# Kernel tuning notes

Hardware: AMD Instinct MI355X
Metric: run time of the kernel (lower is better)

## Reference

```python
import jax, jax.numpy as jnp
import numpy as np

N_BLOCKS = 9
D = 256  # input_dim == edge_dim == hidden_dim
N_NODES = 10000
N_EDGES = 60000
LN_EPS = 1e-5


def _layer_norm(h, g, b):
    m = h.mean(-1, keepdims=True)
    v = ((h - m) ** 2).mean(-1, keepdims=True)
    return (h - m) * jax.lax.rsqrt(v + LN_EPS) * g + b


def _mlp(h, W1, b1, W2, b2, W3, b3, g, beta):
    # Linear->ReLU, Linear->ReLU (hidden_layers=2), Linear, LayerNorm
    h = jax.nn.relu(h @ W1 + b1)
    h = jax.nn.relu(h @ W2 + b2)
    h = h @ W3 + b3
    return _layer_norm(h, g, beta)


def setup_inputs() -> dict:
    key = jax.random.key(0)
    ks = jax.random.split(key, 24)
    x = jax.random.normal(ks[0], (N_NODES, D), jnp.float32)
    edge_index = jax.random.randint(ks[1], (2, N_EDGES), 0, N_NODES, jnp.int32)
    edge_attr = jax.random.normal(ks[2], (N_EDGES, D), jnp.float32)

    def w(k, shape):
        fan_in = shape[-2]
        return jax.random.normal(k, shape, jnp.float32) * (1.0 / np.sqrt(fan_in))

    B = N_BLOCKS
    inp = {"x": x, "edge_index": edge_index, "edge_attr": edge_attr}
    # edge MLP: in 3D -> D -> D -> D, LayerNorm(D)
    inp["eW1"] = w(ks[3], (B, 3 * D, D)); inp["eB1"] = jnp.zeros((B, D), jnp.float32)
    inp["eW2"] = w(ks[4], (B, D, D));     inp["eB2"] = jnp.zeros((B, D), jnp.float32)
    inp["eW3"] = w(ks[5], (B, D, D));     inp["eB3"] = jnp.zeros((B, D), jnp.float32)
    inp["eLNg"] = jnp.ones((B, D), jnp.float32); inp["eLNb"] = jnp.zeros((B, D), jnp.float32)
    # node MLP: in 2D -> D -> D -> D, LayerNorm(D)
    inp["nW1"] = w(ks[6], (B, 2 * D, D)); inp["nB1"] = jnp.zeros((B, D), jnp.float32)
    inp["nW2"] = w(ks[7], (B, D, D));     inp["nB2"] = jnp.zeros((B, D), jnp.float32)
    inp["nW3"] = w(ks[8], (B, D, D));     inp["nB3"] = jnp.zeros((B, D), jnp.float32)
    inp["nLNg"] = jnp.ones((B, D), jnp.float32); inp["nLNb"] = jnp.zeros((B, D), jnp.float32)
    return inp


def reference(x, edge_index, edge_attr,
              eW1, eB1, eW2, eB2, eW3, eB3, eLNg, eLNb,
              nW1, nB1, nW2, nB2, nW3, nB3, nLNg, nLNb):
    src = edge_index[0]
    dst = edge_index[1]
    n_nodes = x.shape[0]

    def block(carry, p):
        xc, ea = carry
        (ew1, eb1, ew2, eb2, ew3, eb3, eg, ebn,
         nw1, nb1, nw2, nb2, nw3, nb3, ng, nbn) = p
        # edge update: gather endpoints, MLP, residual
        msg_in = jnp.concatenate([xc[src], xc[dst], ea], axis=-1)  # [E, 3D]
        ea = ea + _mlp(msg_in, ew1, eb1, ew2, eb2, ew3, eb3, eg, ebn)
        # node update: scatter-sum messages to destination, MLP, residual
        agg = jax.ops.segment_sum(ea, dst, num_segments=n_nodes)  # [N, D]
        node_in = jnp.concatenate([xc, agg], axis=-1)  # [N, 2D]
        xc = xc + _mlp(node_in, nw1, nb1, nw2, nb2, nw3, nb3, ng, nbn)
        return (xc, ea), None

    params = (eW1, eB1, eW2, eB2, eW3, eB3, eLNg, eLNb,
              nW1, nB1, nW2, nB2, nW3, nB3, nLNg, nLNb)
    (x_out, _), _ = jax.lax.scan(block, (x, edge_attr), params)
    return x_out
```

## Files before the change

### kernel.cpp

```cpp
#include <hip/hip_runtime.h>

#define D 256

typedef __attribute__((ext_vector_type(8))) short bf16x8;
typedef __attribute__((ext_vector_type(4))) float f32x4;

__device__ inline unsigned short f2bf(float f) {
  union { float f; unsigned u; } v; v.f = f;
  unsigned r = v.u + 0x7FFFu + ((v.u >> 16) & 1u);
  return (unsigned short)(r >> 16);
}
__device__ inline float bf2f(unsigned short u) {
  union { unsigned u; float f; } v; v.u = ((unsigned)u) << 16;
  return v.f;
}

__device__ inline void gl_lds16(const void* gsrc, void* ldst) {
  __builtin_amdgcn_global_load_lds(
      (const __attribute__((address_space(1))) void*)gsrc,
      (__attribute__((address_space(3))) void*)ldst, 16, 0, 0);
}

__global__ void wprep_kernel(const float* __restrict__ w, unsigned short* __restrict__ wt,
                             int Kfull, int k0, int Ksub, int total) {
  int idx = blockIdx.x * 256 + threadIdx.x;
  if (idx >= total) return;
  int per_b = Ksub * D;
  int b = idx / per_b;
  int r = idx % per_b;
  int j = r & 7;
  int lane = (r >> 3) & 63;
  int t = r >> 9;
  int kt = t >> 4, ct = t & 15;
  int k = kt * 32 + (lane >> 4) * 8 + j;
  int col = ct * 16 + (lane & 15);
  wt[idx] = f2bf(w[((size_t)b * Kfull + k0 + k) * D + col]);
}

__global__ void cvt_bf16_kernel(const float4* __restrict__ in, ushort4* __restrict__ out, int n4) {
  int i = blockIdx.x * 256 + threadIdx.x;
  if (i >= n4) return;
  float4 f = in[i];
  ushort4 o;
  o.x = f2bf(f.x); o.y = f2bf(f.y); o.z = f2bf(f.z); o.w = f2bf(f.w);
  out[i] = o;
}

__global__ void hist_kernel(const int* __restrict__ dst, int* __restrict__ hist, int E) {
  int i = blockIdx.x * 256 + threadIdx.x;
  if (i < E) atomicAdd(&hist[dst[i]], 1);
}

__global__ void scan_kernel(const int* __restrict__ hist, int* __restrict__ offs, int Nn) {
  __shared__ int part[256];
  int t = threadIdx.x;
  int chunk = (Nn + 255) >> 8;
  int s = t * chunk;
  int e = s + chunk; if (e > Nn) e = Nn; if (s > Nn) s = Nn;
  int sum = 0;
  for (int i = s; i < e; ++i) sum += hist[i];
  part[t] = sum;
  __syncthreads();
  if (t == 0) {
    int run = 0;
    for (int i = 0; i < 256; ++i) { int v = part[i]; part[i] = run; run += v; }
  }
  __syncthreads();
  int run = part[t];
  for (int i = s; i < e; ++i) { offs[i] = run; run += hist[i]; }
  if (e == Nn) offs[Nn] = run;
}

__global__ void fill_kernel(const int* __restrict__ dst, const int* __restrict__ offs,
                            int* __restrict__ cnt, int* __restrict__ eid, int E) {
  int i = blockIdx.x * 256 + threadIdx.x;
  if (i < E) {
    int d = dst[i];
    int p = offs[d] + atomicAdd(&cnt[d], 1);
    eid[p] = i;
  }
}

__global__ __launch_bounds__(256) void agg_kernel(
    const unsigned short* __restrict__ eabf, const int* __restrict__ eid,
    const int* __restrict__ offs, unsigned short* __restrict__ aggbf, int Nn) {
  int node = blockIdx.x * 4 + (threadIdx.x >> 6);
  if (node >= Nn) return;
  int lane = threadIdx.x & 63;
  int s = offs[node], e = offs[node + 1];
  float4 acc = make_float4(0.f, 0.f, 0.f, 0.f);
  for (int i = s; i < e; ++i) {
    int ed = eid[i];
    ushort4 v = *(const ushort4*)(eabf + (size_t)ed * D + lane * 4);
    acc.x += bf2f(v.x); acc.y += bf2f(v.y); acc.z += bf2f(v.z); acc.w += bf2f(v.w);
  }
  ushort4 o;
  o.x = f2bf(acc.x); o.y = f2bf(acc.y); o.z = f2bf(acc.z); o.w = f2bf(acc.w);
  *(ushort4*)(aggbf + (size_t)node * D + lane * 4) = o;
}

__global__ __launch_bounds__(256, 4) void gemm32(
    const unsigned short* __restrict__ A, const unsigned short* __restrict__ W,
    unsigned short* __restrict__ out, int M)
{
  const int tid  = threadIdx.x;
  const int lane = tid & 63;
  const int wave = tid >> 6;
  const int lr   = lane & 15;
  const int lq   = lane >> 4;
  const int r0   = blockIdx.x * 32;

  int ro[2];
  #pragma unroll
  for (int mt = 0; mt < 2; ++mt) {
    int rw = r0 + mt * 16 + lr;
    if (rw > M - 1) rw = M - 1;
    ro[mt] = rw * D;
  }
  const int ctb = wave * 4;
  f32x4 acc[2][4];
  #pragma unroll
  for (int i = 0; i < 2; i++)
    #pragma unroll
    for (int j = 0; j < 4; j++)
      acc[i][j] = (f32x4){0.f, 0.f, 0.f, 0.f};

  constexpr int DEPTH = 3;
  bf16x8 afb[DEPTH][2], bqb[DEPTH][4];
  #pragma unroll
  for (int d = 0; d < DEPTH; ++d) {
    #pragma unroll
    for (int mt = 0; mt < 2; ++mt)
      afb[d][mt] = *(const bf16x8*)(A + ro[mt] + (d << 5) + lq * 8);
    #pragma unroll
    for (int nt = 0; nt < 4; ++nt)
      bqb[d][nt] = *(const bf16x8*)(W + (((d * 16 + ctb + nt) * 64 + lane) * 8));
  }
  #pragma unroll
  for (int kt = 0; kt < 8; ++kt) {
    const int s = kt % DEPTH;
    #pragma unroll
    for (int mt = 0; mt < 2; ++mt)
      #pragma unroll
      for (int nt = 0; nt < 4; ++nt)
        acc[mt][nt] = __builtin_amdgcn_mfma_f32_16x16x32_bf16(afb[s][mt], bqb[s][nt], acc[mt][nt], 0, 0, 0);
    if (kt + DEPTH < 8) {
      const int kn = kt + DEPTH;
      #pragma unroll
      for (int mt = 0; mt < 2; ++mt)
        afb[s][mt] = *(const bf16x8*)(A + ro[mt] + (kn << 5) + lq * 8);
      #pragma unroll
      for (int nt = 0; nt < 4; ++nt)
        bqb[s][nt] = *(const bf16x8*)(W + (((kn * 16 + ctb + nt) * 64 + lane) * 8));
    }
  }
  #pragma unroll
  for (int mt = 0; mt < 2; ++mt)
    #pragma unroll
    for (int r = 0; r < 4; ++r) {
      const int row = r0 + mt * 16 + lq * 4 + r;
      if (row < M) {
        #pragma unroll
        for (int nt = 0; nt < 4; ++nt)
          out[(size_t)row * D + wave * 64 + nt * 16 + lr] = f2bf(acc[mt][nt][r]);
      }
    }
}

__global__ __launch_bounds__(256, 4) void fused_edge(
    unsigned short* __restrict__ eabf,
    const int* __restrict__ src, const int* __restrict__ dst,
    const unsigned short* __restrict__ Ubf, const unsigned short* __restrict__ Vbf,
    const unsigned short* __restrict__ W1c, const float* __restrict__ b1,
    const unsigned short* __restrict__ W2, const float* __restrict__ b2,
    const unsigned short* __restrict__ W3, const float* __restrict__ b3,
    const float* __restrict__ lng, const float* __restrict__ lnb, int E)
{
  __shared__ __align__(16) unsigned short SH[16896];
  unsigned short* Us = SH;
  unsigned short* Vs = SH + 8192;
  unsigned short* Hs = SH;
  float* ps1 = (float*)(SH + 16384);
  float* ps2 = (float*)(SH + 16384) + 128;

  const int tid  = threadIdx.x;
  const int lane = tid & 63;
  const int wave = tid >> 6;
  const int lr   = lane & 15;
  const int lq   = lane >> 4;
  const int r0   = blockIdx.x * 32;

  #pragma unroll
  for (int c = 0; c < 4; ++c) {
    int row = wave * 8 + c * 2 + (lane >> 5);
    int er = r0 + row; if (er > E - 1) er = E - 1;
    int colel = (lane & 31) * 8;
    gl_lds16(Ubf + (size_t)src[er] * D + colel, Us + wave * 2048 + c * 512);
    gl_lds16(Vbf + (size_t)dst[er] * D + colel, Vs + wave * 2048 + c * 512);
  }

  int ro[2];
  #pragma unroll
  for (int mt = 0; mt < 2; ++mt) {
    int rw = r0 + mt * 16 + lr;
    if (rw > E - 1) rw = E - 1;
    ro[mt] = rw * D;
  }
  const int ctb = wave * 4;
  #define LOADB(Wp, kt, dst_)                                                 \
    _Pragma("unroll")                                                         \
    for (int nt = 0; nt < 4; ++nt)                                            \
      dst_[nt] = *(const bf16x8*)((Wp) + ((((kt) * 16 + ctb + nt) * 64 + lane) * 8));

  f32x4 acc[2][4];
  constexpr int DEPTH = 3;
  bf16x8 afb[DEPTH][2], bqb[DEPTH][4];

  #pragma unroll
  for (int i = 0; i < 2; i++)
    #pragma unroll
    for (int j = 0; j < 4; j++)
      acc[i][j] = (f32x4){0.f, 0.f, 0.f, 0.f};
  #pragma unroll
  for (int d = 0; d < DEPTH; ++d) {
    #pragma unroll
    for (int mt = 0; mt < 2; ++mt)
      afb[d][mt] = *(const bf16x8*)(eabf + ro[mt] + (d << 5) + lq * 8);
    LOADB(W1c, d, bqb[d]);
  }
  #pragma unroll
  for (int kt = 0; kt < 8; ++kt) {
    const int s = kt % DEPTH;
    #pragma unroll
    for (int mt = 0; mt < 2; ++mt)
      #pragma unroll
      for (int nt = 0; nt < 4; ++nt)
        acc[mt][nt] = __builtin_amdgcn_mfma_f32_16x16x32_bf16(afb[s][mt], bqb[s][nt], acc[mt][nt], 0, 0, 0);
    if (kt + DEPTH < 8) {
      const int kn = kt + DEPTH;
      #pragma unroll
      for (int mt = 0; mt < 2; ++mt)
        afb[s][mt] = *(const bf16x8*)(eabf + ro[mt] + (kn << 5) + lq * 8);
      LOADB(W1c, kn, bqb[s]);
    }
  }
  __syncthreads();

  {
    float bv[4];
    #pragma unroll
    for (int nt = 0; nt < 4; ++nt) bv[nt] = b1[wave * 64 + nt * 16 + lr];
    #pragma unroll
    for (int mt = 0; mt < 2; ++mt)
      #pragma unroll
      for (int r = 0; r < 4; ++r) {
        const int row = mt * 16 + lq * 4 + r;
        #pragma unroll
        for (int nt = 0; nt < 4; ++nt) {
          const int col = wave * 64 + nt * 16 + lr;
          float v = acc[mt][nt][r] + bv[nt]
                  + bf2f(Us[row * 256 + col]) + bf2f(Vs[row * 256 + col]);
          acc[mt][nt][r] = v > 0.f ? v : 0.f;
        }
      }
  }
  __syncthreads();
  #pragma unroll
  for (int mt = 0; mt < 2; ++mt)
    #pragma unroll
    for (int r = 0; r < 4; ++r) {
      const int row = mt * 16 + lq * 4 + r;
      #pragma unroll
      for (int nt = 0; nt < 4; ++nt)
        Hs[row * 264 + wave * 64 + nt * 16 + lr] = f2bf(acc[mt][nt][r]);
    }
  __syncthreads();

  #pragma unroll
  for (int i = 0; i < 2; i++)
    #pragma unroll
    for (int j = 0; j < 4; j++)
      acc[i][j] = (f32x4){0.f, 0.f, 0.f, 0.f};
  #pragma unroll
  for (int d = 0; d < DEPTH; ++d) LOADB(W2, d, bqb[d]);
  #pragma unroll
  for (int kt = 0; kt < 8; ++kt) {
    const int s = kt % DEPTH;
    bf16x8 afc[2];
    #pragma unroll
    for (int mt = 0; mt < 2; ++mt)
      afc[mt] = *(const bf16x8*)&Hs[(mt * 16 + lr) * 264 + (kt << 5) + lq * 8];
    #pragma unroll
    for (int mt = 0; mt < 2; ++mt)
      #pragma unroll
      for (int nt = 0; nt < 4; ++nt)
        acc[mt][nt] = __builtin_amdgcn_mfma_f32_16x16x32_bf16(afc[mt], bqb[s][nt], acc[mt][nt], 0, 0, 0);
    if (kt + DEPTH < 8) LOADB(W2, kt + DEPTH, bqb[s]);
  }
  __syncthreads();
  {
    float bv[4];
    #pragma unroll
    for (int nt = 0; nt < 4; ++nt) bv[nt] = b2[wave * 64 + nt * 16 + lr];
    #pragma unroll
    for (int mt = 0; mt < 2; ++mt)
      #pragma unroll
      for (int r = 0; r < 4; ++r) {
        const int row = mt * 16 + lq * 4 + r;
        #pragma unroll
        for (int nt = 0; nt < 4; ++nt) {
          float v = acc[mt][nt][r] + bv[nt];
          v = v > 0.f ? v : 0.f;
          Hs[row * 264 + wave * 64 + nt * 16 + lr] = f2bf(v);
        }
      }
  }
  __syncthreads();

  #pragma unroll
  for (int i = 0; i < 2; i++)
    #pragma unroll
    for (int j = 0; j < 4; j++)
      acc[i][j] = (f32x4){0.f, 0.f, 0.f, 0.f};
  #pragma unroll
  for (int d = 0; d < DEPTH; ++d) LOADB(W3, d, bqb[d]);
  #pragma unroll
  for (int kt = 0; kt < 8; ++kt) {
    const int s = kt % DEPTH;
    bf16x8 afc[2];
    #pragma unroll
    for (int mt = 0; mt < 2; ++mt)
      afc[mt] = *(const bf16x8*)&Hs[(mt * 16 + lr) * 264 + (kt << 5) + lq * 8];
    #pragma unroll
    for (int mt = 0; mt < 2; ++mt)
      #pragma unroll
      for (int nt = 0; nt < 4; ++nt)
        acc[mt][nt] = __builtin_amdgcn_mfma_f32_16x16x32_bf16(afc[mt], bqb[s][nt], acc[mt][nt], 0, 0, 0);
    if (kt + DEPTH < 8) LOADB(W3, kt + DEPTH, bqb[s]);
  }
  #pragma unroll
  for (int nt = 0; nt < 4; ++nt) {
    const float bv = b3[wave * 64 + nt * 16 + lr];
    #pragma unroll
    for (int mt = 0; mt < 2; ++mt)
      #pragma unroll
      for (int r = 0; r < 4; ++r)
        acc[mt][nt][r] += bv;
  }
  #pragma unroll
  for (int mt = 0; mt < 2; ++mt) {
    #pragma unroll
    for (int r = 0; r < 4; ++r) {
      float s1 = 0.f, s2 = 0.f;
      #pragma unroll
      for (int nt = 0; nt < 4; ++nt) {
        float v = acc[mt][nt][r];
        s1 += v; s2 += v * v;
      }
      #pragma unroll
      for (int dlt = 1; dlt < 16; dlt <<= 1) {
        s1 += __shfl_xor(s1, dlt, 64);
        s2 += __shfl_xor(s2, dlt, 64);
      }
      if (lr == 0) {
        ps1[(mt * 16 + lq * 4 + r) * 4 + wave] = s1;
        ps2[(mt * 16 + lq * 4 + r) * 4 + wave] = s2;
      }
    }
  }
  __syncthreads();
  #pragma unroll
  for (int mt = 0; mt < 2; ++mt) {
    #pragma unroll
    for (int r = 0; r < 4; ++r) {
      const int rl = mt * 16 + lq * 4 + r;
      const int row = r0 + rl;
      float fs1 = ps1[rl * 4 + 0] + ps1[rl * 4 + 1] + ps1[rl * 4 + 2] + ps1[rl * 4 + 3];
      float fs2 = ps2[rl * 4 + 0] + ps2[rl * 4 + 1] + ps2[rl * 4 + 2] + ps2[rl * 4 + 3];
      float mean = fs1 * (1.f / 256.f);
      float var  = fs2 * (1.f / 256.f) - mean * mean;
      float rstd = rsqrtf(var + 1e-5f);
      if (row < E) {
        #pragma unroll
        for (int nt = 0; nt < 4; ++nt) {
          const int col = wave * 64 + nt * 16 + lr;
          float v = (acc[mt][nt][r] - mean) * rstd * lng[col] + lnb[col];
          unsigned short* bp = eabf + (size_t)row * D + col;
          *bp = f2bf(bf2f(*bp) + v);
        }
      }
    }
  }
  #undef LOADB
}

template<int NCHUNK>
__global__ __launch_bounds__(256, 4) void fused_mlp(
    const unsigned short* __restrict__ C0, const int* __restrict__ g0,
    const unsigned short* __restrict__ C1, const int* __restrict__ g1,
    const unsigned short* __restrict__ C2,
    const unsigned short* __restrict__ W1, const float* __restrict__ b1,
    const unsigned short* __restrict__ W2, const float* __restrict__ b2,
    const unsigned short* __restrict__ W3, const float* __restrict__ b3,
    const float* __restrict__ lng, const float* __restrict__ lnb,
    float* __restrict__ resid, unsigned short* __restrict__ bfout, int M)
{
  __shared__ __align__(16) unsigned short Hs[32 * 264];
  __shared__ float ps1[128];
  __shared__ float ps2[128];

  const int tid  = threadIdx.x;
  const int lane = tid & 63;
  const int wave = tid >> 6;
  const int lr   = lane & 15;
  const int lq   = lane >> 4;
  const int r0   = blockIdx.x * 32;

  int ro0[2], ro1[2], ro2[2];
  #pragma unroll
  for (int mt = 0; mt < 2; ++mt) {
    int rw = r0 + mt * 16 + lr;
    if (rw > M - 1) rw = M - 1;
    ro0[mt] = (g0 ? g0[rw] : rw) * D;
    ro1[mt] = (NCHUNK > 1) ? ((g1 ? g1[rw] : rw) * D) : 0;
    ro2[mt] = (NCHUNK > 2) ? rw * D : 0;
  }

  f32x4 acc[2][4];
  const int ctb = wave * 4;
  #define LOADB(Wp, kt, dst)                                                  \
    _Pragma("unroll")                                                         \
    for (int nt = 0; nt < 4; ++nt)                                            \
      dst[nt] = *(const bf16x8*)((Wp) + ((((kt) * 16 + ctb + nt) * 64 + lane) * 8));
  #define LOADA(kt, dst) {                                                    \
    const int c_ = (kt) >> 3;                                                 \
    const int koff_ = (((kt) & 7) << 5) + lq * 8;                             \
    const unsigned short* bp_ = (c_ == 0) ? C0 : (c_ == 1 ? C1 : C2);         \
    _Pragma("unroll")                                                         \
    for (int mt = 0; mt < 2; ++mt) {                                          \
      int r_ = ro0[mt];                                                       \
      if (NCHUNK > 1 && c_ == 1) r_ = ro1[mt];                                \
      if (NCHUNK > 2 && c_ == 2) r_ = ro2[mt];                                \
      dst[mt] = *(const bf16x8*)(bp_ + r_ + koff_);                           \
    }                                                                         \
  }

  constexpr int DEPTH = 3;
  bf16x8 afb[DEPTH][2], bqb[DEPTH][4];

  #pragma unroll
  for (int i = 0; i < 2; i++)
    #pragma unroll
    for (int j = 0; j < 4; j++)
      acc[i][j] = (f32x4){0.f, 0.f, 0.f, 0.f};

  constexpr int NKT = NCHUNK * 8;
  #pragma unroll
  for (int d = 0; d < DEPTH; ++d) {
    LOADA(d, afb[d]);
    LOADB(W1, d, bqb[d]);
  }
  #pragma unroll
  for (int kt = 0; kt < NKT; ++kt) {
    const int s = kt % DEPTH;
    #pragma unroll
    for (int mt = 0; mt < 2; ++mt)
      #pragma unroll
      for (int nt = 0; nt < 4; ++nt)
        acc[mt][nt] = __builtin_amdgcn_mfma_f32_16x16x32_bf16(afb[s][mt], bqb[s][nt], acc[mt][nt], 0, 0, 0);
    if (kt + DEPTH < NKT) {
      LOADA(kt + DEPTH, afb[s]);
      LOADB(W1, kt + DEPTH, bqb[s]);
    }
  }
  {
    float bv[4];
    #pragma unroll
    for (int nt = 0; nt < 4; ++nt) bv[nt] = b1[wave * 64 + nt * 16 + lr];
    #pragma unroll
    for (int mt = 0; mt < 2; ++mt)
      #pragma unroll
      for (int r = 0; r < 4; ++r) {
        const int row = mt * 16 + lq * 4 + r;
        #pragma unroll
        for (int nt = 0; nt < 4; ++nt) {
          float v = acc[mt][nt][r] + bv[nt];
          v = v > 0.f ? v : 0.f;
          Hs[row * 264 + wave * 64 + nt * 16 + lr] = f2bf(v);
        }
      }
  }
  __syncthreads();

  #pragma unroll
  for (int i = 0; i < 2; i++)
    #pragma unroll
    for (int j = 0; j < 4; j++)
      acc[i][j] = (f32x4){0.f, 0.f, 0.f, 0.f};
  #pragma unroll
  for (int d = 0; d < DEPTH; ++d) LOADB(W2, d, bqb[d]);
  #pragma unroll
  for (int kt = 0; kt < 8; ++kt) {
    const int s = kt % DEPTH;
    bf16x8 afc[2];
    #pragma unroll
    for (int mt = 0; mt < 2; ++mt)
      afc[mt] = *(const bf16x8*)&Hs[(mt * 16 + lr) * 264 + (kt << 5) + lq * 8];
    #pragma unroll
    for (int mt = 0; mt < 2; ++mt)
      #pragma unroll
      for (int nt = 0; nt < 4; ++nt)
        acc[mt][nt] = __builtin_amdgcn_mfma_f32_16x16x32_bf16(afc[mt], bqb[s][nt], acc[mt][nt], 0, 0, 0);
    if (kt + DEPTH < 8) LOADB(W2, kt + DEPTH, bqb[s]);
  }
  __syncthreads();
  {
    float bv[4];
    #pragma unroll
    for (int nt = 0; nt < 4; ++nt) bv[nt] = b2[wave * 64 + nt * 16 + lr];
    #pragma unroll
    for (int mt = 0; mt < 2; ++mt)
      #pragma unroll
      for (int r = 0; r < 4; ++r) {
        const int row = mt * 16 + lq * 4 + r;
        #pragma unroll
        for (int nt = 0; nt < 4; ++nt) {
          float v = acc[mt][nt][r] + bv[nt];
          v = v > 0.f ? v : 0.f;
          Hs[row * 264 + wave * 64 + nt * 16 + lr] = f2bf(v);
        }
      }
  }
  __syncthreads();

  #pragma unroll
  for (int i = 0; i < 2; i++)
    #pragma unroll
    for (int j = 0; j < 4; j++)
      acc[i][j] = (f32x4){0.f, 0.f, 0.f, 0.f};
  #pragma unroll
  for (int d = 0; d < DEPTH; ++d) LOADB(W3, d, bqb[d]);
  #pragma unroll
  for (int kt = 0; kt < 8; ++kt) {
    const int s = kt % DEPTH;
    bf16x8 afc[2];
    #pragma unroll
    for (int mt = 0; mt < 2; ++mt)
      afc[mt] = *(const bf16x8*)&Hs[(mt * 16 + lr) * 264 + (kt << 5) + lq * 8];
    #pragma unroll
    for (int mt = 0; mt < 2; ++mt)
      #pragma unroll
      for (int nt = 0; nt < 4; ++nt)
        acc[mt][nt] = __builtin_amdgcn_mfma_f32_16x16x32_bf16(afc[mt], bqb[s][nt], acc[mt][nt], 0, 0, 0);
    if (kt + DEPTH < 8) LOADB(W3, kt + DEPTH, bqb[s]);
  }
  #pragma unroll
  for (int nt = 0; nt < 4; ++nt) {
    const float bv = b3[wave * 64 + nt * 16 + lr];
    #pragma unroll
    for (int mt = 0; mt < 2; ++mt)
      #pragma unroll
      for (int r = 0; r < 4; ++r)
        acc[mt][nt][r] += bv;
  }
  #pragma unroll
  for (int mt = 0; mt < 2; ++mt) {
    #pragma unroll
    for (int r = 0; r < 4; ++r) {
      float s1 = 0.f, s2 = 0.f;
      #pragma unroll
      for (int nt = 0; nt < 4; ++nt) {
        float v = acc[mt][nt][r];
        s1 += v; s2 += v * v;
      }
      #pragma unroll
      for (int dlt = 1; dlt < 16; dlt <<= 1) {
        s1 += __shfl_xor(s1, dlt, 64);
        s2 += __shfl_xor(s2, dlt, 64);
      }
      if (lr == 0) {
        ps1[(mt * 16 + lq * 4 + r) * 4 + wave] = s1;
        ps2[(mt * 16 + lq * 4 + r) * 4 + wave] = s2;
      }
    }
  }
  __syncthreads();
  #pragma unroll
  for (int mt = 0; mt < 2; ++mt) {
    #pragma unroll
    for (int r = 0; r < 4; ++r) {
      const int rl = mt * 16 + lq * 4 + r;
      const int row = r0 + rl;
      float fs1 = ps1[rl * 4 + 0] + ps1[rl * 4 + 1] + ps1[rl * 4 + 2] + ps1[rl * 4 + 3];
      float fs2 = ps2[rl * 4 + 0] + ps2[rl * 4 + 1] + ps2[rl * 4 + 2] + ps2[rl * 4 + 3];
      float mean = fs1 * (1.f / 256.f);
      float var  = fs2 * (1.f / 256.f) - mean * mean;
      float rstd = rsqrtf(var + 1e-5f);
      if (row < M) {
        #pragma unroll
        for (int nt = 0; nt < 4; ++nt) {
          const int col = wave * 64 + nt * 16 + lr;
          float v = (acc[mt][nt][r] - mean) * rstd * lng[col] + lnb[col];
          if (resid) {
            float* rp = resid + (size_t)row * D + col;
            float nv = *rp + v;
            *rp = nv;
            if (bfout) bfout[(size_t)row * D + col] = f2bf(nv);
          } else {
            unsigned short* bp = bfout + (size_t)row * D + col;
            *bp = f2bf(bf2f(*bp) + v);
          }
        }
      }
    }
  }
  #undef LOADA
  #undef LOADB
}

extern "C" void kernel_launch(void* const* d_in, const int* in_sizes, int n_in,
                              void* d_out, int out_size, void* d_ws, size_t ws_size,
                              hipStream_t stream) {
  const float* x         = (const float*)d_in[0];
  const int*   eidx      = (const int*)d_in[1];
  const float* edge_attr = (const float*)d_in[2];
  const float* eW1 = (const float*)d_in[3];
  const float* eB1 = (const float*)d_in[4];
  const float* eW2 = (const float*)d_in[5];
  const float* eB2 = (const float*)d_in[6];
  const float* eW3 = (const float*)d_in[7];
  const float* eB3 = (const float*)d_in[8];
  const float* eLNg = (const float*)d_in[9];
  const float* eLNb = (const float*)d_in[10];
  const float* nW1 = (const float*)d_in[11];
  const float* nB1 = (const float*)d_in[12];
  const float* nW2 = (const float*)d_in[13];
  const float* nB2 = (const float*)d_in[14];
  const float* nW3 = (const float*)d_in[15];
  const float* nB3 = (const float*)d_in[16];
  const float* nLNg = (const float*)d_in[17];
  const float* nLNb = (const float*)d_in[18];

  const int Nn = in_sizes[0] / D;
  const int E  = in_sizes[1] / 2;
  const int B  = in_sizes[4] / D;

  const int* srcI = eidx;
  const int* dstI = eidx + E;

  char* wsp = (char*)d_ws;
  size_t off = 0;
  auto alloc = [&](size_t bytes) {
    char* p = wsp + off;
    off += (bytes + 255) & ~(size_t)255;
    return p;
  };
  unsigned short* eW1at = (unsigned short*)alloc((size_t)B * 256 * D * 2);
  unsigned short* eW1bt = (unsigned short*)alloc((size_t)B * 256 * D * 2);
  unsigned short* eW1ct = (unsigned short*)alloc((size_t)B * 256 * D * 2);
  unsigned short* eW2t  = (unsigned short*)alloc((size_t)B * 256 * D * 2);
  unsigned short* eW3t  = (unsigned short*)alloc((size_t)B * 256 * D * 2);
  unsigned short* nW1t  = (unsigned short*)alloc((size_t)B * 512 * D * 2);
  unsigned short* nW2t  = (unsigned short*)alloc((size_t)B * 256 * D * 2);
  unsigned short* nW3t  = (unsigned short*)alloc((size_t)B * 256 * D * 2);
  unsigned short* eabf  = (unsigned short*)alloc((size_t)E * D * 2);
  unsigned short* xbf   = (unsigned short*)alloc((size_t)Nn * D * 2);
  unsigned short* aggbf = (unsigned short*)alloc((size_t)Nn * D * 2);
  unsigned short* Ubf   = (unsigned short*)alloc((size_t)Nn * D * 2);
  unsigned short* Vbf   = (unsigned short*)alloc((size_t)Nn * D * 2);
  int*            hist  = (int*)alloc((size_t)(Nn + 1) * 4);
  int*            offs  = (int*)alloc((size_t)(Nn + 1) * 4);
  int*            cnt   = (int*)alloc((size_t)Nn * 4);
  int*            eid   = (int*)alloc((size_t)E * 4);

  float* xbuf = (float*)d_out;

  auto wp = [&](const float* w, unsigned short* wt, int Kfull, int k0, int Ksub) {
    int total = B * Ksub * D;
    wprep_kernel<<<(total + 255) / 256, 256, 0, stream>>>(w, wt, Kfull, k0, Ksub, total);
  };
  wp(eW1, eW1at, 768, 0, 256);
  wp(eW1, eW1bt, 768, 256, 256);
  wp(eW1, eW1ct, 768, 512, 256);
  wp(eW2, eW2t, 256, 0, 256);
  wp(eW3, eW3t, 256, 0, 256);
  wp(nW1, nW1t, 512, 0, 512);
  wp(nW2, nW2t, 256, 0, 256);
  wp(nW3, nW3t, 256, 0, 256);

  hipMemcpyAsync(xbuf, x, (size_t)Nn * D * 4, hipMemcpyDeviceToDevice, stream);
  {
    int n4 = E * D / 4;
    cvt_bf16_kernel<<<(n4 + 255) / 256, 256, 0, stream>>>(
        (const float4*)edge_attr, (ushort4*)eabf, n4);
    int m4 = Nn * D / 4;
    cvt_bf16_kernel<<<(m4 + 255) / 256, 256, 0, stream>>>(
        (const float4*)x, (ushort4*)xbf, m4);
  }

  hipMemsetAsync(hist, 0, (size_t)Nn * 4, stream);
  hipMemsetAsync(cnt, 0, (size_t)Nn * 4, stream);
  hist_kernel<<<(E + 255) / 256, 256, 0, stream>>>(dstI, hist, E);
  scan_kernel<<<1, 256, 0, stream>>>(hist, offs, Nn);
  fill_kernel<<<(E + 255) / 256, 256, 0, stream>>>(dstI, offs, cnt, eid, E);

  const int gridE = (E + 31) / 32;
  const int gridN = (Nn + 31) / 32;
  const int gridA = (Nn + 3) / 4;

  for (int b = 0; b < B; ++b) {
    gemm32<<<gridN, 256, 0, stream>>>(xbf, eW1at + (size_t)b * 256 * D, Ubf, Nn);
    gemm32<<<gridN, 256, 0, stream>>>(xbf, eW1bt + (size_t)b * 256 * D, Vbf, Nn);
    fused_edge<<<gridE, 256, 0, stream>>>(
        eabf, srcI, dstI, Ubf, Vbf,
        eW1ct + (size_t)b * 256 * D, eB1 + b * D,
        eW2t + (size_t)b * 256 * D, eB2 + b * D,
        eW3t + (size_t)b * 256 * D, eB3 + b * D,
        eLNg + b * D, eLNb + b * D, E);
    agg_kernel<<<gridA, 256, 0, stream>>>(eabf, eid, offs, aggbf, Nn);
    fused_mlp<2><<<gridN, 256, 0, stream>>>(
        xbf, nullptr, aggbf, nullptr, nullptr,
        nW1t + (size_t)b * 512 * D, nB1 + b * D,
        nW2t + (size_t)b * 256 * D, nB2 + b * D,
        nW3t + (size_t)b * 256 * D, nB3 + b * D,
        nLNg + b * D, nLNb + b * D, xbuf, xbf, Nn);
  }
}
```

Baseline: 1.384 ms.

## Merge U/V GEMMs, shrink node tiles to 16 rows, stage edge attrs in LDS

The two per-block node GEMMs for U and V become one launch that picks the weight and output by block index. The node GEMMs and the node MLP now use 16-row tiles, doubling grid size to improve occupancy on the 10k-node problem. The edge kernel stages its edge-attribute tile into padded LDS with coalesced loads and reads A fragments from there. Its residual update now goes through LDS and is written back with vectorized 16-byte stores instead of scattered 2-byte read-modify-writes. In exchange the edge kernel uses more LDS, which may lower occupancy, and the smaller node tiles reuse each weight load across fewer rows.

```diff
diff --git a/kernel.cpp b/kernel.cpp
--- a/kernel.cpp
+++ b/kernel.cpp
@@ -99,39 +99,35 @@
   *(ushort4*)(aggbf + (size_t)node * D + lane * 4) = o;
 }
 
-__global__ __launch_bounds__(256, 4) void gemm32(
-    const unsigned short* __restrict__ A, const unsigned short* __restrict__ W,
-    unsigned short* __restrict__ out, int M)
+__global__ __launch_bounds__(256, 4) void gemm_uv(
+    const unsigned short* __restrict__ A,
+    const unsigned short* __restrict__ Wa, const unsigned short* __restrict__ Wb,
+    unsigned short* __restrict__ U, unsigned short* __restrict__ V, int M)
 {
+  const int u    = blockIdx.x & 1;
+  const int r0   = (blockIdx.x >> 1) * 16;
+  const unsigned short* W = u ? Wb : Wa;
+  unsigned short* out = u ? V : U;
+
   const int tid  = threadIdx.x;
   const int lane = tid & 63;
   const int wave = tid >> 6;
   const int lr   = lane & 15;
   const int lq   = lane >> 4;
-  const int r0   = blockIdx.x * 32;
-
-  int ro[2];
-  #pragma unroll
-  for (int mt = 0; mt < 2; ++mt) {
-    int rw = r0 + mt * 16 + lr;
-    if (rw > M - 1) rw = M - 1;
-    ro[mt] = rw * D;
-  }
+
+  int rw = r0 + lr; if (rw > M - 1) rw = M - 1;
+  const int ro = rw * D;
   const int ctb = wave * 4;
-  f32x4 acc[2][4];
-  #pragma unroll
-  for (int i = 0; i < 2; i++)
-    #pragma unroll
-    for (int j = 0; j < 4; j++)
-      acc[i][j] = (f32x4){0.f, 0.f, 0.f, 0.f};
+
+  f32x4 acc[4];
+  #pragma unroll
+  for (int j = 0; j < 4; j++) acc[j] = (f32x4){0.f, 0.f, 0.f, 0.f};
 
   constexpr int DEPTH = 3;
-  bf16x8 afb[DEPTH][2], bqb[DEPTH][4];
+  bf16x8 afb[DEPTH], bqb[DEPTH][4];
   #pragma unroll
   for (int d = 0; d < DEPTH; ++d) {
-    #pragma unroll
-    for (int mt = 0; mt < 2; ++mt)
-      afb[d][mt] = *(const bf16x8*)(A + ro[mt] + (d << 5) + lq * 8);
+    afb[d] = *(const bf16x8*)(A + ro + (d << 5) + lq * 8);
     #pragma unroll
     for (int nt = 0; nt < 4; ++nt)
       bqb[d][nt] = *(const bf16x8*)(W + (((d * 16 + ctb + nt) * 64 + lane) * 8));
@@ -140,31 +136,25 @@
   for (int kt = 0; kt < 8; ++kt) {
     const int s = kt % DEPTH;
     #pragma unroll
-    for (int mt = 0; mt < 2; ++mt)
-      #pragma unroll
-      for (int nt = 0; nt < 4; ++nt)
-        acc[mt][nt] = __builtin_amdgcn_mfma_f32_16x16x32_bf16(afb[s][mt], bqb[s][nt], acc[mt][nt], 0, 0, 0);
+    for (int nt = 0; nt < 4; ++nt)
+      acc[nt] = __builtin_amdgcn_mfma_f32_16x16x32_bf16(afb[s], bqb[s][nt], acc[nt], 0, 0, 0);
     if (kt + DEPTH < 8) {
       const int kn = kt + DEPTH;
-      #pragma unroll
-      for (int mt = 0; mt < 2; ++mt)
-        afb[s][mt] = *(const bf16x8*)(A + ro[mt] + (kn << 5) + lq * 8);
+      afb[s] = *(const bf16x8*)(A + ro + (kn << 5) + lq * 8);
       #pragma unroll
       for (int nt = 0; nt < 4; ++nt)
         bqb[s][nt] = *(const bf16x8*)(W + (((kn * 16 + ctb + nt) * 64 + lane) * 8));
     }
   }
   #pragma unroll
-  for (int mt = 0; mt < 2; ++mt)
-    #pragma unroll
-    for (int r = 0; r < 4; ++r) {
-      const int row = r0 + mt * 16 + lq * 4 + r;
-      if (row < M) {
-        #pragma unroll
-        for (int nt = 0; nt < 4; ++nt)
-          out[(size_t)row * D + wave * 64 + nt * 16 + lr] = f2bf(acc[mt][nt][r]);
-      }
-    }
+  for (int r = 0; r < 4; ++r) {
+    const int row = r0 + lq * 4 + r;
+    if (row < M) {
+      #pragma unroll
+      for (int nt = 0; nt < 4; ++nt)
+        out[(size_t)row * D + wave * 64 + nt * 16 + lr] = f2bf(acc[nt][r]);
+    }
+  }
 }
 
 __global__ __launch_bounds__(256, 4) void fused_edge(
@@ -176,12 +166,13 @@
     const unsigned short* __restrict__ W3, const float* __restrict__ b3,
     const float* __restrict__ lng, const float* __restrict__ lnb, int E)
 {
-  __shared__ __align__(16) unsigned short SH[16896];
-  unsigned short* Us = SH;
-  unsigned short* Vs = SH + 8192;
-  unsigned short* Hs = SH;
-  float* ps1 = (float*)(SH + 16384);
-  float* ps2 = (float*)(SH + 16384) + 128;
+  __shared__ __align__(16) unsigned short SH[24832];
+  unsigned short* eaS = SH;
+  unsigned short* Hs  = SH;
+  unsigned short* Us  = SH + 8448;
+  unsigned short* Vs  = SH + 8448 + 8192;
+  float* ps1 = (float*)(SH + 8448);
+  float* ps2 = (float*)(SH + 8448) + 128;
 
   const int tid  = threadIdx.x;
   const int lane = tid & 63;
@@ -191,6 +182,16 @@
   const int r0   = blockIdx.x * 32;
 
   #pragma unroll
+  for (int i = 0; i < 4; ++i) {
+    int row = i * 8 + (tid >> 5);
+    int cs  = (tid & 31) * 8;
+    int er = r0 + row; if (er > E - 1) er = E - 1;
+    uint4 v = *(const uint4*)(eabf + (size_t)er * D + cs);
+    *(uint4*)&eaS[row * 264 + cs] = v;
+  }
+  __syncthreads();
+
+  #pragma unroll
   for (int c = 0; c < 4; ++c) {
     int row = wave * 8 + c * 2 + (lane >> 5);
     int er = r0 + row; if (er > E - 1) er = E - 1;
@@ -199,13 +200,6 @@
     gl_lds16(Vbf + (size_t)dst[er] * D + colel, Vs + wave * 2048 + c * 512);
   }
 
-  int ro[2];
-  #pragma unroll
-  for (int mt = 0; mt < 2; ++mt) {
-    int rw = r0 + mt * 16 + lr;
-    if (rw > E - 1) rw = E - 1;
-    ro[mt] = rw * D;
-  }
   const int ctb = wave * 4;
   #define LOADB(Wp, kt, dst_)                                                 \
     _Pragma("unroll")                                                         \
@@ -214,7 +208,7 @@
 
   f32x4 acc[2][4];
   constexpr int DEPTH = 3;
-  bf16x8 afb[DEPTH][2], bqb[DEPTH][4];
+  bf16x8 bqb[DEPTH][4];
 
   #pragma unroll
   for (int i = 0; i < 2; i++)
@@ -222,27 +216,20 @@
     for (int j = 0; j < 4; j++)
       acc[i][j] = (f32x4){0.f, 0.f, 0.f, 0.f};
   #pragma unroll
-  for (int d = 0; d < DEPTH; ++d) {
-    #pragma unroll
-    for (int mt = 0; mt < 2; ++mt)
-      afb[d][mt] = *(const bf16x8*)(eabf + ro[mt] + (d << 5) + lq * 8);
-    LOADB(W1c, d, bqb[d]);
-  }
+  for (int d = 0; d < DEPTH; ++d) LOADB(W1c, d, bqb[d]);
   #pragma unroll
   for (int kt = 0; kt < 8; ++kt) {
     const int s = kt % DEPTH;
+    bf16x8 afc[2];
+    #pragma unroll
+    for (int mt = 0; mt < 2; ++mt)
+      afc[mt] = *(const bf16x8*)&eaS[(mt * 16 + lr) * 264 + (kt << 5) + lq * 8];
     #pragma unroll
     for (int mt = 0; mt < 2; ++mt)
       #pragma unroll
       for (int nt = 0; nt < 4; ++nt)
-        acc[mt][nt] = __builtin_amdgcn_mfma_f32_16x16x32_bf16(afb[s][mt], bqb[s][nt], acc[mt][nt], 0, 0, 0);
-    if (kt + DEPTH < 8) {
-      const int kn = kt + DEPTH;
-      #pragma unroll
-      for (int mt = 0; mt < 2; ++mt)
-        afb[s][mt] = *(const bf16x8*)(eabf + ro[mt] + (kn << 5) + lq * 8);
-      LOADB(W1c, kn, bqb[s]);
-    }
+        acc[mt][nt] = __builtin_amdgcn_mfma_f32_16x16x32_bf16(afc[mt], bqb[s][nt], acc[mt][nt], 0, 0, 0);
+    if (kt + DEPTH < 8) LOADB(W1c, kt + DEPTH, bqb[s]);
   }
   __syncthreads();
 
@@ -374,103 +361,90 @@
     #pragma unroll
     for (int r = 0; r < 4; ++r) {
       const int rl = mt * 16 + lq * 4 + r;
-      const int row = r0 + rl;
       float fs1 = ps1[rl * 4 + 0] + ps1[rl * 4 + 1] + ps1[rl * 4 + 2] + ps1[rl * 4 + 3];
       float fs2 = ps2[rl * 4 + 0] + ps2[rl * 4 + 1] + ps2[rl * 4 + 2] + ps2[rl * 4 + 3];
       float mean = fs1 * (1.f / 256.f);
       float var  = fs2 * (1.f / 256.f) - mean * mean;
       float rstd = rsqrtf(var + 1e-5f);
-      if (row < E) {
-        #pragma unroll
-        for (int nt = 0; nt < 4; ++nt) {
-          const int col = wave * 64 + nt * 16 + lr;
-          float v = (acc[mt][nt][r] - mean) * rstd * lng[col] + lnb[col];
-          unsigned short* bp = eabf + (size_t)row * D + col;
-          *bp = f2bf(bf2f(*bp) + v);
-        }
-      }
+      #pragma unroll
+      for (int nt = 0; nt < 4; ++nt) {
+        const int col = wave * 64 + nt * 16 + lr;
+        float v = (acc[mt][nt][r] - mean) * rstd * lng[col] + lnb[col];
+        Hs[rl * 264 + col] = f2bf(v);
+      }
+    }
+  }
+  __syncthreads();
+  #pragma unroll
+  for (int i = 0; i < 4; ++i) {
+    int row = i * 8 + (tid >> 5);
+    int cs  = (tid & 31) * 8;
+    int er = r0 + row;
+    if (er < E) {
+      uint4 dv = *(const uint4*)&Hs[row * 264 + cs];
+      uint4 ov = *(const uint4*)(eabf + (size_t)er * D + cs);
+      const unsigned short* dp = (const unsigned short*)&dv;
+      const unsigned short* op = (const unsigned short*)&ov;
+      uint4 res;
+      unsigned short* rp = (unsigned short*)&res;
+      #pragma unroll
+      for (int j = 0; j < 8; ++j) rp[j] = f2bf(bf2f(op[j]) + bf2f(dp[j]));
+      *(uint4*)(eabf + (size_t)er * D + cs) = res;
     }
   }
   #undef LOADB
 }
 
-template<int NCHUNK>
-__global__ __launch_bounds__(256, 4) void fused_mlp(
-    const unsigned short* __restrict__ C0, const int* __restrict__ g0,
-    const unsigned short* __restrict__ C1, const int* __restrict__ g1,
-    const unsigned short* __restrict__ C2,
+__global__ __launch_bounds__(256, 4) void fused_node(
+    const unsigned short* __restrict__ xbf, const unsigned short* __restrict__ aggbf,
     const unsigned short* __restrict__ W1, const float* __restrict__ b1,
     const unsigned short* __restrict__ W2, const float* __restrict__ b2,
     const unsigned short* __restrict__ W3, const float* __restrict__ b3,
     const float* __restrict__ lng, const float* __restrict__ lnb,
     float* __restrict__ resid, unsigned short* __restrict__ bfout, int M)
 {
-  __shared__ __align__(16) unsigned short Hs[32 * 264];
-  __shared__ float ps1[128];
-  __shared__ float ps2[128];
+  __shared__ __align__(16) unsigned short Hs[16 * 264];
+  __shared__ float ps1[64];
+  __shared__ float ps2[64];
 
   const int tid  = threadIdx.x;
   const int lane = tid & 63;
   const int wave = tid >> 6;
   const int lr   = lane & 15;
   const int lq   = lane >> 4;
-  const int r0   = blockIdx.x * 32;
-
-  int ro0[2], ro1[2], ro2[2];
-  #pragma unroll
-  for (int mt = 0; mt < 2; ++mt) {
-    int rw = r0 + mt * 16 + lr;
-    if (rw > M - 1) rw = M - 1;
-    ro0[mt] = (g0 ? g0[rw] : rw) * D;
-    ro1[mt] = (NCHUNK > 1) ? ((g1 ? g1[rw] : rw) * D) : 0;
-    ro2[mt] = (NCHUNK > 2) ? rw * D : 0;
-  }
-
-  f32x4 acc[2][4];
+  const int r0   = blockIdx.x * 16;
+
+  int rw = r0 + lr; if (rw > M - 1) rw = M - 1;
+  const int ro = rw * D;
   const int ctb = wave * 4;
-  #define LOADB(Wp, kt, dst)                                                  \
+
+  #define LOADB(Wp, kt, dst_)                                                 \
     _Pragma("unroll")                                                         \
     for (int nt = 0; nt < 4; ++nt)                                            \
-      dst[nt] = *(const bf16x8*)((Wp) + ((((kt) * 16 + ctb + nt) * 64 + lane) * 8));
-  #define LOADA(kt, dst) {                                                    \
-    const int c_ = (kt) >> 3;                                                 \
-    const int koff_ = (((kt) & 7) << 5) + lq * 8;                             \
-    const unsigned short* bp_ = (c_ == 0) ? C0 : (c_ == 1 ? C1 : C2);         \
-    _Pragma("unroll")                                                         \
-    for (int mt = 0; mt < 2; ++mt) {                                          \
-      int r_ = ro0[mt];                                                       \
-      if (NCHUNK > 1 && c_ == 1) r_ = ro1[mt];                                \
-      if (NCHUNK > 2 && c_ == 2) r_ = ro2[mt];                                \
-      dst[mt] = *(const bf16x8*)(bp_ + r_ + koff_);                           \
-    }                                                                         \
-  }
-
+      dst_[nt] = *(const bf16x8*)((Wp) + ((((kt) * 16 + ctb + nt) * 64 + lane) * 8));
+
+  f32x4 acc[4];
   constexpr int DEPTH = 3;
-  bf16x8 afb[DEPTH][2], bqb[DEPTH][4];
-
-  #pragma unroll
-  for (int i = 0; i < 2; i++)
-    #pragma unroll
-    for (int j = 0; j < 4; j++)
-      acc[i][j] = (f32x4){0.f, 0.f, 0.f, 0.f};
-
-  constexpr int NKT = NCHUNK * 8;
+  bf16x8 afb[DEPTH], bqb[DEPTH][4];
+
+  #pragma unroll
+  for (int j = 0; j < 4; j++) acc[j] = (f32x4){0.f, 0.f, 0.f, 0.f};
   #pragma unroll
   for (int d = 0; d < DEPTH; ++d) {
-    LOADA(d, afb[d]);
+    afb[d] = *(const bf16x8*)(xbf + ro + (d << 5) + lq * 8);
     LOADB(W1, d, bqb[d]);
   }
   #pragma unroll
-  for (int kt = 0; kt < NKT; ++kt) {
+  for (int kt = 0; kt < 16; ++kt) {
     const int s = kt % DEPTH;
     #pragma unroll
-    for (int mt = 0; mt < 2; ++mt)
-      #pragma unroll
-      for (int nt = 0; nt < 4; ++nt)
-        acc[mt][nt] = __builtin_amdgcn_mfma_f32_16x16x32_bf16(afb[s][mt], bqb[s][nt], acc[mt][nt], 0, 0, 0);
-    if (kt + DEPTH < NKT) {
-      LOADA(kt + DEPTH, afb[s]);
-      LOADB(W1, kt + DEPTH, bqb[s]);
+    for (int nt = 0; nt < 4; ++nt)
+      acc[nt] = __builtin_amdgcn_mfma_f32_16x16x32_bf16(afb[s], bqb[s][nt], acc[nt], 0, 0, 0);
+    if (kt + DEPTH < 16) {
+      const int kn = kt + DEPTH;
+      const unsigned short* bp = (kn < 8) ? xbf : aggbf;
+      afb[s] = *(const bf16x8*)(bp + ro + ((kn & 7) << 5) + lq * 8);
+      LOADB(W1, kn, bqb[s]);
     }
   }
   {
@@ -478,39 +452,29 @@
     #pragma unroll
     for (int nt = 0; nt < 4; ++nt) bv[nt] = b1[wave * 64 + nt * 16 + lr];
     #pragma unroll
-    for (int mt = 0; mt < 2; ++mt)
-      #pragma unroll
-      for (int r = 0; r < 4; ++r) {
-        const int row = mt * 16 + lq * 4 + r;
-        #pragma unroll
-        for (int nt = 0; nt < 4; ++nt) {
-          float v = acc[mt][nt][r] + bv[nt];
-          v = v > 0.f ? v : 0.f;
-          Hs[row * 264 + wave * 64 + nt * 16 + lr] = f2bf(v);
-        }
-      }
-  }
-  __syncthreads();
-
-  #pragma unroll
-  for (int i = 0; i < 2; i++)
-    #pragma unroll
-    for (int j = 0; j < 4; j++)
-      acc[i][j] = (f32x4){0.f, 0.f, 0.f, 0.f};
+    for (int r = 0; r < 4; ++r) {
+      const int row = lq * 4 + r;
+      #pragma unroll
+      for (int nt = 0; nt < 4; ++nt) {
+        float v = acc[nt][r] + bv[nt];
+        v = v > 0.f ? v : 0.f;
+        Hs[row * 264 + wave * 64 + nt * 16 + lr] = f2bf(v);
+      }
+    }
+  }
+  __syncthreads();
+
+  #pragma unroll
+  for (int j = 0; j < 4; j++) acc[j] = (f32x4){0.f, 0.f, 0.f, 0.f};
   #pragma unroll
   for (int d = 0; d < DEPTH; ++d) LOADB(W2, d, bqb[d]);
   #pragma unroll
   for (int kt = 0; kt < 8; ++kt) {
     const int s = kt % DEPTH;
-    bf16x8 afc[2];
-    #pragma unroll
-    for (int mt = 0; mt < 2; ++mt)
-      afc[mt] = *(const bf16x8*)&Hs[(mt * 16 + lr) * 264 + (kt << 5) + lq * 8];
-    #pragma unroll
-    for (int mt = 0; mt < 2; ++mt)
-      #pragma unroll
-      for (int nt = 0; nt < 4; ++nt)
-        acc[mt][nt] = __builtin_amdgcn_mfma_f32_16x16x32_bf16(afc[mt], bqb[s][nt], acc[mt][nt], 0, 0, 0);
+    bf16x8 afc = *(const bf16x8*)&Hs[lr * 264 + (kt << 5) + lq * 8];
+    #pragma unroll
+    for (int nt = 0; nt < 4; ++nt)
+      acc[nt] = __builtin_amdgcn_mfma_f32_16x16x32_bf16(afc, bqb[s][nt], acc[nt], 0, 0, 0);
     if (kt + DEPTH < 8) LOADB(W2, kt + DEPTH, bqb[s]);
   }
   __syncthreads();
@@ -519,102 +483,77 @@
     #pragma unroll
     for (int nt = 0; nt < 4; ++nt) bv[nt] = b2[wave * 64 + nt * 16 + lr];
     #pragma unroll
-    for (int mt = 0; mt < 2; ++mt)
-      #pragma unroll
-      for (int r = 0; r < 4; ++r) {
-        const int row = mt * 16 + lq * 4 + r;
-        #pragma unroll
-        for (int nt = 0; nt < 4; ++nt) {
-          float v = acc[mt][nt][r] + bv[nt];
-          v = v > 0.f ? v : 0.f;
-          Hs[row * 264 + wave * 64 + nt * 16 + lr] = f2bf(v);
-        }
-      }
-  }
-  __syncthreads();
-
-  #pragma unroll
-  for (int i = 0; i < 2; i++)
-    #pragma unroll
-    for (int j = 0; j < 4; j++)
-      acc[i][j] = (f32x4){0.f, 0.f, 0.f, 0.f};
+    for (int r = 0; r < 4; ++r) {
+      const int row = lq * 4 + r;
+      #pragma unroll
+      for (int nt = 0; nt < 4; ++nt) {
+        float v = acc[nt][r] + bv[nt];
+        v = v > 0.f ? v : 0.f;
+        Hs[row * 264 + wave * 64 + nt * 16 + lr] = f2bf(v);
+      }
+    }
+  }
+  __syncthreads();
+
+  #pragma unroll
+  for (int j = 0; j < 4; j++) acc[j] = (f32x4){0.f, 0.f, 0.f, 0.f};
   #pragma unroll
   for (int d = 0; d < DEPTH; ++d) LOADB(W3, d, bqb[d]);
   #pragma unroll
   for (int kt = 0; kt < 8; ++kt) {
     const int s = kt % DEPTH;
-    bf16x8 afc[2];
-    #pragma unroll
-    for (int mt = 0; mt < 2; ++mt)
-      afc[mt] = *(const bf16x8*)&Hs[(mt * 16 + lr) * 264 + (kt << 5) + lq * 8];
-    #pragma unroll
-    for (int mt = 0; mt < 2; ++mt)
-      #pragma unroll
-      for (int nt = 0; nt < 4; ++nt)
-        acc[mt][nt] = __builtin_amdgcn_mfma_f32_16x16x32_bf16(afc[mt], bqb[s][nt], acc[mt][nt], 0, 0, 0);
+    bf16x8 afc = *(const bf16x8*)&Hs[lr * 264 + (kt << 5) + lq * 8];
+    #pragma unroll
+    for (int nt = 0; nt < 4; ++nt)
+      acc[nt] = __builtin_amdgcn_mfma_f32_16x16x32_bf16(afc, bqb[s][nt], acc[nt], 0, 0, 0);
     if (kt + DEPTH < 8) LOADB(W3, kt + DEPTH, bqb[s]);
   }
   #pragma unroll
   for (int nt = 0; nt < 4; ++nt) {
     const float bv = b3[wave * 64 + nt * 16 + lr];
     #pragma unroll
-    for (int mt = 0; mt < 2; ++mt)
-      #pragma unroll
-      for (int r = 0; r < 4; ++r)
-        acc[mt][nt][r] += bv;
-  }
-  #pragma unroll
-  for (int mt = 0; mt < 2; ++mt) {
-    #pragma unroll
-    for (int r = 0; r < 4; ++r) {
-      float s1 = 0.f, s2 = 0.f;
+    for (int r = 0; r < 4; ++r) acc[nt][r] += bv;
+  }
+  #pragma unroll
+  for (int r = 0; r < 4; ++r) {
+    float s1 = 0.f, s2 = 0.f;
+    #pragma unroll
+    for (int nt = 0; nt < 4; ++nt) {
+      float v = acc[nt][r];
+      s1 += v; s2 += v * v;
+    }
+    #pragma unroll
+    for (int dlt = 1; dlt < 16; dlt <<= 1) {
+      s1 += __shfl_xor(s1, dlt, 64);
+      s2 += __shfl_xor(s2, dlt, 64);
+    }
+    if (lr == 0) {
+      ps1[(lq * 4 + r) * 4 + wave] = s1;
+      ps2[(lq * 4 + r) * 4 + wave] = s2;
+    }
+  }
+  __syncthreads();
+  #pragma unroll
+  for (int r = 0; r < 4; ++r) {
+    const int rl = lq * 4 + r;
+    const int row = r0 + rl;
+    float fs1 = ps1[rl * 4 + 0] + ps1[rl * 4 + 1] + ps1[rl * 4 + 2] + ps1[rl * 4 + 3];
+    float fs2 = ps2[rl * 4 + 0] + ps2[rl * 4 + 1] + ps2[rl * 4 + 2] + ps2[rl * 4 + 3];
+    float mean = fs1 * (1.f / 256.f);
+    float var  = fs2 * (1.f / 256.f) - mean * mean;
+    float rstd = rsqrtf(var + 1e-5f);
+    if (row < M) {
       #pragma unroll
       for (int nt = 0; nt < 4; ++nt) {
-        float v = acc[mt][nt][r];
-        s1 += v; s2 += v * v;
-      }
-      #pragma unroll
-      for (int dlt = 1; dlt < 16; dlt <<= 1) {
-        s1 += __shfl_xor(s1, dlt, 64);
-        s2 += __shfl_xor(s2, dlt, 64);
-      }
-      if (lr == 0) {
-        ps1[(mt * 16 + lq * 4 + r) * 4 + wave] = s1;
-        ps2[(mt * 16 + lq * 4 + r) * 4 + wave] = s2;
-      }
-    }
-  }
-  __syncthreads();
-  #pragma unroll
-  for (int mt = 0; mt < 2; ++mt) {
-    #pragma unroll
-    for (int r = 0; r < 4; ++r) {
-      const int rl = mt * 16 + lq * 4 + r;
-      const int row = r0 + rl;
-      float fs1 = ps1[rl * 4 + 0] + ps1[rl * 4 + 1] + ps1[rl * 4 + 2] + ps1[rl * 4 + 3];
-      float fs2 = ps2[rl * 4 + 0] + ps2[rl * 4 + 1] + ps2[rl * 4 + 2] + ps2[rl * 4 + 3];
-      float mean = fs1 * (1.f / 256.f);
-      float var  = fs2 * (1.f / 256.f) - mean * mean;
-      float rstd = rsqrtf(var + 1e-5f);
-      if (row < M) {
-        #pragma unroll
-        for (int nt = 0; nt < 4; ++nt) {
-          const int col = wave * 64 + nt * 16 + lr;
-          float v = (acc[mt][nt][r] - mean) * rstd * lng[col] + lnb[col];
-          if (resid) {
-            float* rp = resid + (size_t)row * D + col;
-            float nv = *rp + v;
-            *rp = nv;
-            if (bfout) bfout[(size_t)row * D + col] = f2bf(nv);
-          } else {
-            unsigned short* bp = bfout + (size_t)row * D + col;
-            *bp = f2bf(bf2f(*bp) + v);
-          }
-        }
-      }
-    }
-  }
-  #undef LOADA
+        const int col = wave * 64 + nt * 16 + lr;
+        float v = (acc[nt][r] - mean) * rstd * lng[col] + lnb[col];
+        float* rp = resid + (size_t)row * D + col;
+        float nv = *rp + v;
+        *rp = nv;
+        bfout[(size_t)row * D + col] = f2bf(nv);
+      }
+    }
+  }
   #undef LOADB
 }
 
@@ -704,13 +643,14 @@
   scan_kernel<<<1, 256, 0, stream>>>(hist, offs, Nn);
   fill_kernel<<<(E + 255) / 256, 256, 0, stream>>>(dstI, offs, cnt, eid, E);
 
-  const int gridE = (E + 31) / 32;
-  const int gridN = (Nn + 31) / 32;
-  const int gridA = (Nn + 3) / 4;
+  const int gridE  = (E + 31) / 32;
+  const int gridN  = (Nn + 15) / 16;
+  const int gridUV = gridN * 2;
+  const int gridA  = (Nn + 3) / 4;
 
   for (int b = 0; b < B; ++b) {
-    gemm32<<<gridN, 256, 0, stream>>>(xbf, eW1at + (size_t)b * 256 * D, Ubf, Nn);
-    gemm32<<<gridN, 256, 0, stream>>>(xbf, eW1bt + (size_t)b * 256 * D, Vbf, Nn);
+    gemm_uv<<<gridUV, 256, 0, stream>>>(
+        xbf, eW1at + (size_t)b * 256 * D, eW1bt + (size_t)b * 256 * D, Ubf, Vbf, Nn);
     fused_edge<<<gridE, 256, 0, stream>>>(
         eabf, srcI, dstI, Ubf, Vbf,
         eW1ct + (size_t)b * 256 * D, eB1 + b * D,
@@ -718,8 +658,8 @@
         eW3t + (size_t)b * 256 * D, eB3 + b * D,
         eLNg + b * D, eLNb + b * D, E);
     agg_kernel<<<gridA, 256, 0, stream>>>(eabf, eid, offs, aggbf, Nn);
-    fused_mlp<2><<<gridN, 256, 0, stream>>>(
-        xbf, nullptr, aggbf, nullptr, nullptr,
+    fused_node<<<gridN, 256, 0, stream>>>(
+        xbf, aggbf,
         nW1t + (size_t)b * 512 * D, nB1 + b * D,
         nW2t + (size_t)b * 256 * D, nB2 + b * D,
         nW3t + (size_t)b * 256 * D, nB3 + b * D,
```

Result: faster. 1.228 ms (-11.3%).
